# Performance work log

Measured on AMD Instinct MI355X. Metric: run time of the kernel, lower is better.

Reference implementation:

```python
import jax, jax.numpy as jnp
import numpy as np

NUM_HEADS = 8
WINDOW = 5
DILATION = 1


def _offsets(window, dilation):
    r = dilation * (window // 2)
    return [(dy, dx) for dy in range(-r, r + 1, dilation)
            for dx in range(-r, r + 1, dilation)]


def _neighbors(x, window, dilation):
    # x: [B, heads, head_dim, Hc, Wc] -> [B, heads, K, head_dim, Hc, Wc]
    B, Hn, hd, Hc, Wc = x.shape
    r = dilation * (window // 2)
    xp = jnp.pad(x, ((0, 0), (0, 0), (0, 0), (r, r), (r, r)))
    offs = _offsets(window, dilation)
    return jnp.stack(
        [xp[..., r + dy:r + dy + Hc, r + dx:r + dx + Wc] for dy, dx in offs],
        axis=2)


def _valid_mask(Hc, Wc, window, dilation):
    # [K, Hc, Wc] bool: True where the shifted neighbor lies inside the map
    ys = jnp.arange(Hc)
    xs = jnp.arange(Wc)
    offs = _offsets(window, dilation)
    return jnp.stack(
        [(((ys + dy) >= 0) & ((ys + dy) < Hc))[:, None]
         & (((xs + dx) >= 0) & ((xs + dx) < Wc))[None, :]
         for dy, dx in offs], axis=0)


def _align_to_query_grid(t, out_h, out_w, scale):
    # repeat coarse lattice onto the fine query grid via anchor indexing
    y = jnp.clip(jnp.arange(out_h) // scale, 0, t.shape[-2] - 1)
    x = jnp.clip(jnp.arange(out_w) // scale, 0, t.shape[-1] - 1)
    return jnp.take(jnp.take(t, y, axis=-2), x, axis=-1)


def setup_inputs() -> dict:
    key = jax.random.key(0)
    k1, k2 = jax.random.split(key)
    k = jax.random.normal(k1, (2, 128, 48, 48), dtype=jnp.float32)
    v = jax.random.normal(k2, (2, 128, 48, 48), dtype=jnp.float32)
    return {"k": k, "v": v, "query_height": 96, "query_width": 96,
            "scale_factor": 2}


def reference(k, v, query_height, query_width, scale_factor):
    B, C, Hc, Wc = k.shape
    hd = C // NUM_HEADS
    kh = k.reshape(B, NUM_HEADS, hd, Hc, Wc)
    vh = v.reshape(B, NUM_HEADS, hd, Hc, Wc)
    k_nb = _neighbors(kh, WINDOW, DILATION)  # [B,H,K,hd,Hc,Wc]
    v_nb = _neighbors(vh, WINDOW, DILATION)
    mask = _valid_mask(Hc, Wc, WINDOW, DILATION)  # [K,Hc,Wc]
    K = mask.shape[0]
    mask = jnp.broadcast_to(mask[None, None], (B, NUM_HEADS, K, Hc, Wc))
    k_nb = _align_to_query_grid(k_nb, query_height, query_width, scale_factor)
    v_nb = _align_to_query_grid(v_nb, query_height, query_width, scale_factor)
    mask = _align_to_query_grid(mask, query_height, query_width, scale_factor)
    return (k_nb, v_nb, mask)
```

## Files before the change

kernel.cpp:

```cpp
#include <hip/hip_runtime.h>


#define KV_ELEMS  58982400LL
#define MASK_OFF  117964800LL

typedef float f32x4 __attribute__((ext_vector_type(4)));

__global__ __launch_bounds__(256) void fused_expand_kernel(
    const float* __restrict__ k, const float* __restrict__ v,
    float* __restrict__ out_k, float* __restrict__ out_v,
    float* __restrict__ out_m) {
    const int t  = blockIdx.x * 256 + threadIdx.x;
    const int kk = blockIdx.y;
    const int z  = blockIdx.z;

    const int q  = t / 24;
    const int x4 = t - q * 24;
    const int d  = q / 96;
    const int y  = q - d * 96;

    const int kq = kk / 5;
    const int dy = kq - 2;
    const int dx = kk - kq * 5 - 2;

    const int yy  = (y >> 1) + dy;
    const bool vy = (unsigned)yy < 48u;
    const int xc0 = 2 * x4 + dx;
    const int xc1 = xc0 + 1;
    const bool v0 = vy && ((unsigned)xc0 < 48u);
    const bool v1 = vy && ((unsigned)xc1 < 48u);

    const int yc = vy ? yy : 0;
    const int x0 = min(max(xc0, 0), 47);
    const int x1 = min(max(xc1, 0), 47);

    const int base = ((z * 16 + d) * 48 + yc) * 48;
    float k0 = k[base + x0];
    float k1 = k[base + x1];
    float w0 = v[base + x0];
    float w1 = v[base + x1];
    k0 = v0 ? k0 : 0.0f;
    k1 = v1 ? k1 : 0.0f;
    w0 = v0 ? w0 : 0.0f;
    w1 = v1 ? w1 : 0.0f;

    const int slice = z * 25 + kk;
    const int o = slice * 36864 + t;
    f32x4 ok = {k0, k0, k1, k1};
    f32x4 ov = {w0, w0, w1, w1};
    __builtin_nontemporal_store(ok, reinterpret_cast<f32x4*>(out_k) + o);
    __builtin_nontemporal_store(ov, reinterpret_cast<f32x4*>(out_v) + o);

    if (blockIdx.x < 9) {
        const float m0 = v0 ? 1.0f : 0.0f;
        const float m1 = v1 ? 1.0f : 0.0f;
        f32x4 om = {m0, m0, m1, m1};
        __builtin_nontemporal_store(
            om, reinterpret_cast<f32x4*>(out_m) + slice * 2304 + t);
    }
}

extern "C" void kernel_launch(void* const* d_in, const int* in_sizes, int n_in,
                              void* d_out, int out_size, void* d_ws, size_t ws_size,
                              hipStream_t stream) {
    const float* k = (const float*)d_in[0];
    const float* v = (const float*)d_in[1];
    float* out = (float*)d_out;
    float* out_k = out;
    float* out_v = out + KV_ELEMS;
    float* out_m = out + MASK_OFF;

    fused_expand_kernel<<<dim3(144, 25, 16), 256, 0, stream>>>(
        k, v, out_k, out_v, out_m);
}
```

Measured before the change: 468.2 us.

## Loop over batch-head slices per thread to reuse index and mask math

Replaces the 3D grid with a 1D grid of 1800 blocks. Each thread now loops over 16 slices and handles two heads per iteration, so index, validity and mask computation is done once and reused. Mask stores come from the d0==0 threads within the loop. This reduces grid size and redundant integer work, at the cost of fewer concurrent blocks and longer per-thread store streams in a kernel bound by write bandwidth.

```diff
diff --git a/kernel.cpp b/kernel.cpp
--- a/kernel.cpp
+++ b/kernel.cpp
@@ -6,18 +6,16 @@
 
 typedef float f32x4 __attribute__((ext_vector_type(4)));
 
-__global__ __launch_bounds__(256) void fused_expand_kernel(
-    const float* __restrict__ k, const float* __restrict__ v,
+__global__ __launch_bounds__(256) void sweep_kernel(
+    const float* __restrict__ kp, const float* __restrict__ vp,
     float* __restrict__ out_k, float* __restrict__ out_v,
     float* __restrict__ out_m) {
-    const int t  = blockIdx.x * 256 + threadIdx.x;
-    const int kk = blockIdx.y;
-    const int z  = blockIdx.z;
-
-    const int q  = t / 24;
-    const int x4 = t - q * 24;
-    const int d  = q / 96;
-    const int y  = q - d * 96;
+    const int tid = blockIdx.x * 256 + threadIdx.x;
+    const int x4 = tid % 24;
+    int t = tid / 24;
+    const int y  = t % 96;  t /= 96;
+    const int d0 = t % 8;
+    const int kk = t / 8;
 
     const int kq = kk / 5;
     const int dy = kq - 2;
@@ -26,37 +24,52 @@
     const int yy  = (y >> 1) + dy;
     const bool vy = (unsigned)yy < 48u;
     const int xc0 = 2 * x4 + dx;
-    const int xc1 = xc0 + 1;
     const bool v0 = vy && ((unsigned)xc0 < 48u);
-    const bool v1 = vy && ((unsigned)xc1 < 48u);
+    const bool v1 = vy && ((unsigned)(xc0 + 1) < 48u);
 
     const int yc = vy ? yy : 0;
     const int x0 = min(max(xc0, 0), 47);
-    const int x1 = min(max(xc1, 0), 47);
+    const int x1 = min(max(xc0 + 1, 0), 47);
 
-    const int base = ((z * 16 + d) * 48 + yc) * 48;
-    float k0 = k[base + x0];
-    float k1 = k[base + x1];
-    float w0 = v[base + x0];
-    float w1 = v[base + x1];
-    k0 = v0 ? k0 : 0.0f;
-    k1 = v1 ? k1 : 0.0f;
-    w0 = v0 ? w0 : 0.0f;
-    w1 = v1 ? w1 : 0.0f;
+    int base = (d0 * 48 + yc) * 48;
+    int o = tid + kk * 18432;
 
-    const int slice = z * 25 + kk;
-    const int o = slice * 36864 + t;
-    f32x4 ok = {k0, k0, k1, k1};
-    f32x4 ov = {w0, w0, w1, w1};
-    __builtin_nontemporal_store(ok, reinterpret_cast<f32x4*>(out_k) + o);
-    __builtin_nontemporal_store(ov, reinterpret_cast<f32x4*>(out_v) + o);
-
-    if (blockIdx.x < 9) {
+    const bool do_mask = (d0 == 0);
+    const int mbase = tid - kk * 16128;
+    f32x4 om;
+    if (do_mask) {
         const float m0 = v0 ? 1.0f : 0.0f;
         const float m1 = v1 ? 1.0f : 0.0f;
-        f32x4 om = {m0, m0, m1, m1};
-        __builtin_nontemporal_store(
-            om, reinterpret_cast<f32x4*>(out_m) + slice * 2304 + t);
+        om = (f32x4){m0, m0, m1, m1};
+    }
+
+#pragma unroll 2
+    for (int z = 0; z < 16; ++z) {
+        const int b1 = base;
+        const int b2 = base + 18432;
+        float ka0 = kp[b1 + x0], ka1 = kp[b1 + x1];
+        float kb0 = kp[b2 + x0], kb1 = kp[b2 + x1];
+        float va0 = vp[b1 + x0], va1 = vp[b1 + x1];
+        float vb0 = vp[b2 + x0], vb1 = vp[b2 + x1];
+        ka0 = v0 ? ka0 : 0.0f;  ka1 = v1 ? ka1 : 0.0f;
+        kb0 = v0 ? kb0 : 0.0f;  kb1 = v1 ? kb1 : 0.0f;
+        va0 = v0 ? va0 : 0.0f;  va1 = v1 ? va1 : 0.0f;
+        vb0 = v0 ? vb0 : 0.0f;  vb1 = v1 ? vb1 : 0.0f;
+
+        f32x4 oka = {ka0, ka0, ka1, ka1};
+        f32x4 okb = {kb0, kb0, kb1, kb1};
+        f32x4 ova = {va0, va0, va1, va1};
+        f32x4 ovb = {vb0, vb0, vb1, vb1};
+        __builtin_nontemporal_store(oka, reinterpret_cast<f32x4*>(out_k) + o);
+        __builtin_nontemporal_store(okb, reinterpret_cast<f32x4*>(out_k) + o + 18432);
+        __builtin_nontemporal_store(ova, reinterpret_cast<f32x4*>(out_v) + o);
+        __builtin_nontemporal_store(ovb, reinterpret_cast<f32x4*>(out_v) + o + 18432);
+        if (do_mask)
+            __builtin_nontemporal_store(
+                om, reinterpret_cast<f32x4*>(out_m) + mbase + z * 57600);
+
+        base += 36864;
+        o += 921600;
     }
 }
 
@@ -70,6 +83,5 @@
     float* out_v = out + KV_ELEMS;
     float* out_m = out + MASK_OFF;
 
-    fused_expand_kernel<<<dim3(144, 25, 16), 256, 0, stream>>>(
-        k, v, out_k, out_v, out_m);
+    sweep_kernel<<<1800, 256, 0, stream>>>(k, v, out_k, out_v, out_m);
 }
```

Result: slower. 495.1 us (+5.8%).

## Replace 3D grid with linear sweep over whole output buffer

Applied to the files above, without the earlier changes.

Each thread now writes one float4 of a single flat output index, so consecutive blocks stream sequentially through k, then v, then mask regions instead of each thread writing two far-apart k/v locations plus a mask. This aims to make the write stream more sequential and DRAM-friendly. In exchange it adds more integer div/mod index math per output and doubles the thread count.

```diff
diff --git a/kernel.cpp b/kernel.cpp
--- a/kernel.cpp
+++ b/kernel.cpp
@@ -1,62 +1,65 @@
 #include <hip/hip_runtime.h>
 
 
-#define KV_ELEMS  58982400LL
-#define MASK_OFF  117964800LL
+#define KV_F4    14745600
+#define TOT_F4   30412800
 
 typedef float f32x4 __attribute__((ext_vector_type(4)));
 
-__global__ __launch_bounds__(256) void fused_expand_kernel(
-    const float* __restrict__ k, const float* __restrict__ v,
-    float* __restrict__ out_k, float* __restrict__ out_v,
-    float* __restrict__ out_m) {
-    const int t  = blockIdx.x * 256 + threadIdx.x;
-    const int kk = blockIdx.y;
-    const int z  = blockIdx.z;
+__global__ __launch_bounds__(256) void linear_sweep_kernel(
+    const float* __restrict__ kp, const float* __restrict__ vp,
+    float* __restrict__ out) {
+    const int f = blockIdx.x * 256 + threadIdx.x;
 
-    const int q  = t / 24;
-    const int x4 = t - q * 24;
-    const int d  = q / 96;
-    const int y  = q - d * 96;
+    if (f < 2 * KV_F4) {
+        const bool is_k = (f < KV_F4);
+        const float* __restrict__ src = is_k ? kp : vp;
+        const int f2 = is_k ? f : f - KV_F4;
+        const int x4 = f2 % 24;  int t = f2 / 24;
+        const int y  = t % 96;   t /= 96;
+        const int d  = t % 16;   t /= 16;
+        const int kk = t % 25;   t /= 25;
+        const int kq = kk / 5;
+        const int dy = kq - 2;
+        const int dx = kk - kq * 5 - 2;
 
-    const int kq = kk / 5;
-    const int dy = kq - 2;
-    const int dx = kk - kq * 5 - 2;
+        const int yy  = (y >> 1) + dy;
+        const bool vy = (unsigned)yy < 48u;
+        const int xc0 = 2 * x4 + dx;
+        const int xc1 = xc0 + 1;
+        const bool v0 = vy && ((unsigned)xc0 < 48u);
+        const bool v1 = vy && ((unsigned)xc1 < 48u);
 
-    const int yy  = (y >> 1) + dy;
-    const bool vy = (unsigned)yy < 48u;
-    const int xc0 = 2 * x4 + dx;
-    const int xc1 = xc0 + 1;
-    const bool v0 = vy && ((unsigned)xc0 < 48u);
-    const bool v1 = vy && ((unsigned)xc1 < 48u);
+        const int yc = vy ? yy : 0;
+        const int x0 = min(max(xc0, 0), 47);
+        const int x1 = min(max(xc1, 0), 47);
 
-    const int yc = vy ? yy : 0;
-    const int x0 = min(max(xc0, 0), 47);
-    const int x1 = min(max(xc1, 0), 47);
+        const int base = ((t * 16 + d) * 48 + yc) * 48;
+        float a0 = src[base + x0];
+        float a1 = src[base + x1];
+        a0 = v0 ? a0 : 0.0f;
+        a1 = v1 ? a1 : 0.0f;
+        f32x4 o4 = {a0, a0, a1, a1};
+        __builtin_nontemporal_store(o4, reinterpret_cast<f32x4*>(out) + f);
+    } else {
+        const int f2 = f - 2 * KV_F4;
+        const int x4 = f2 % 24;  int t = f2 / 24;
+        const int y  = t % 96;   t /= 96;
+        const int kk = t % 25;
+        const int kq = kk / 5;
+        const int dy = kq - 2;
+        const int dx = kk - kq * 5 - 2;
 
-    const int base = ((z * 16 + d) * 48 + yc) * 48;
-    float k0 = k[base + x0];
-    float k1 = k[base + x1];
-    float w0 = v[base + x0];
-    float w1 = v[base + x1];
-    k0 = v0 ? k0 : 0.0f;
-    k1 = v1 ? k1 : 0.0f;
-    w0 = v0 ? w0 : 0.0f;
-    w1 = v1 ? w1 : 0.0f;
+        const int yy  = (y >> 1) + dy;
+        const bool vy = (unsigned)yy < 48u;
+        const int xc0 = 2 * x4 + dx;
+        const bool v0 = vy && ((unsigned)xc0 < 48u);
+        const bool v1 = vy && ((unsigned)(xc0 + 1) < 48u);
 
-    const int slice = z * 25 + kk;
-    const int o = slice * 36864 + t;
-    f32x4 ok = {k0, k0, k1, k1};
-    f32x4 ov = {w0, w0, w1, w1};
-    __builtin_nontemporal_store(ok, reinterpret_cast<f32x4*>(out_k) + o);
-    __builtin_nontemporal_store(ov, reinterpret_cast<f32x4*>(out_v) + o);
-
-    if (blockIdx.x < 9) {
         const float m0 = v0 ? 1.0f : 0.0f;
         const float m1 = v1 ? 1.0f : 0.0f;
-        f32x4 om = {m0, m0, m1, m1};
-        __builtin_nontemporal_store(
-            om, reinterpret_cast<f32x4*>(out_m) + slice * 2304 + t);
+        f32x4 o4 = {m0, m0, m1, m1};
+        __builtin_nontemporal_store(o4, reinterpret_cast<f32x4*>(out) + f);
     }
 }
 
@@ -66,10 +69,6 @@
     const float* k = (const float*)d_in[0];
     const float* v = (const float*)d_in[1];
     float* out = (float*)d_out;
-    float* out_k = out;
-    float* out_v = out + KV_ELEMS;
-    float* out_m = out + MASK_OFF;
 
-    fused_expand_kernel<<<dim3(144, 25, 16), 256, 0, stream>>>(
-        k, v, out_k, out_v, out_m);
+    linear_sweep_kernel<<<118800, 256, 0, stream>>>(k, v, out);
 }
```

Result: slower. 488.0 us (+4.2%).
